# Kernel tuning notes

Hardware: AMD Instinct MI355X
Metric: run time of the kernel (lower is better)

## Reference

```python
import jax, jax.numpy as jnp
import numpy as np

W, L, D = 4096, 32, 256
WORD_VOCAB, CHR_VOCAB = 50000, 128


def conv1d(x, w, b):
    # x: [N, C_in, T], w: [C_out, C_in, 3], padding=1 (same)
    y = jax.lax.conv_general_dilated(
        x, w, window_strides=(1,), padding=[(1, 1)],
        dimension_numbers=("NCW", "OIW", "NCW"))
    return y + b[None, :, None]


def setup_inputs() -> dict:
    key = jax.random.key(0)
    ks = jax.random.split(key, 12)
    words = jax.random.randint(ks[0], (W,), 0, WORD_VOCAB, dtype=jnp.int32)
    words_in_char = jax.random.randint(ks[1], (W, L), 0, CHR_VOCAB, dtype=jnp.int32)
    s = 0.02
    word_emb = (jax.random.normal(ks[2], (WORD_VOCAB, D), jnp.float32) * s).at[0].set(0.0)  # padding_idx=0
    chr_emb = (jax.random.normal(ks[3], (CHR_VOCAB, D), jnp.float32) * s).at[0].set(0.0)
    conv_chr_w = jax.random.normal(ks[4], (D, D, 3), jnp.float32) * s
    conv_chr_b = jax.random.normal(ks[5], (D,), jnp.float32) * s
    conv_sent_w = jax.random.normal(ks[6], (2 * D, 2 * D, 3), jnp.float32) * s
    conv_sent_b = jax.random.normal(ks[7], (2 * D,), jnp.float32) * s
    w1 = jax.random.normal(ks[8], (4 * D, 2 * D), jnp.float32) * s
    b1 = jax.random.normal(ks[9], (4 * D,), jnp.float32) * s
    w2 = jax.random.normal(ks[10], (2, 4 * D), jnp.float32) * s
    b2 = jax.random.normal(ks[11], (2,), jnp.float32) * s
    return dict(words=words, words_in_char=words_in_char,
                word_emb=word_emb, chr_emb=chr_emb,
                conv_chr_w=conv_chr_w, conv_chr_b=conv_chr_b,
                conv_sent_w=conv_sent_w, conv_sent_b=conv_sent_b,
                w1=w1, b1=b1, w2=w2, b2=b2)


def reference(words, words_in_char, word_emb, chr_emb,
              conv_chr_w, conv_chr_b, conv_sent_w, conv_sent_b,
              w1, b1, w2, b2):
    # word embeddings: [W, D]
    vector_wrds = word_emb[words]
    # char path, batched over all words (equivalent to the per-word loop):
    ch = chr_emb[words_in_char]                      # [W, L, D]
    ch = jnp.transpose(ch, (0, 2, 1))                # [W, D, L]
    wc = conv1d(ch, conv_chr_w, conv_chr_b)          # [W, D, L]
    vector_wchs = jnp.max(wc, axis=2)                # [W, D]
    # sentence conv over the word axis
    u = jnp.concatenate([vector_wrds, vector_wchs], axis=1)  # [W, 2D]
    u = u.T[None, :, :]                              # [1, 2D, W]
    r = conv1d(u, conv_sent_w, conv_sent_b)          # [1, 2D, W]
    r = jnp.max(r, axis=2)                           # [1, 2D]
    h = jnp.tanh(r @ w1.T + b1)                      # [1, 4D]
    return h @ w2.T + b2                             # [1, 2]
```

## Files before the change

kernel.cpp:

```cpp
#include <hip/hip_runtime.h>
#include <hip/hip_bf16.h>
#include <math.h>

#define NW 4096
#define NL 32
#define ND 256
#define ND2 512

typedef __attribute__((ext_vector_type(8))) short short8;
typedef __attribute__((ext_vector_type(4))) float floatx4;

__device__ inline float bitsf(unsigned u) {
  union { unsigned u; float f; } v;
  v.u = u;
  return v.f;
}


__global__ __launch_bounds__(256) void prep_table_kernel(
    const float* __restrict__ conv_sent_w, const float* __restrict__ conv_chr_w,
    const float* __restrict__ chr_emb, __hip_bfloat16* __restrict__ Wb,
    __hip_bfloat16* __restrict__ Tb, short* __restrict__ u_base) {
  __shared__ float s_w[256][49];
  __shared__ float s_e[2][256];
  const int b = blockIdx.x;
  const int tid = threadIdx.x;
  if (b >= 64) {
    if (b < 3136) {
      int idx = (b - 64) * 256 + tid;
      float v = conv_sent_w[idx];
      int co = idx / 1536;
      int rem = idx - co * 1536;
      int ci = rem / 3;
      int k = rem - ci * 3;
      Wb[k * 262144 + co * 512 + ci] = __float2bfloat16(v);
    } else {
      u_base[tid] = 0; u_base[tid + 256] = 0;
      u_base[4097 * 512 + tid] = 0; u_base[4097 * 512 + tid + 256] = 0;
    }
    return;
  }
  const int c0 = b * 2;
  const int co = tid;
  s_e[0][tid] = chr_emb[(c0 + 0) * 256 + tid];
  s_e[1][tid] = chr_emb[(c0 + 1) * 256 + tid];
  float acc[2][3] = {};
  for (int chk = 0; chk < 16; ++chk) {
    const int ci0 = chk * 16;
    __syncthreads();
#pragma unroll 8
    for (int i = 0; i < 48; ++i) {
      int f = tid + i * 256;
      int wco = f / 48;
      int j = f - wco * 48;
      s_w[wco][j] = conv_chr_w[wco * 768 + ci0 * 3 + j];
    }
    __syncthreads();
#pragma unroll
    for (int ci = 0; ci < 16; ++ci) {
      float t_w0 = s_w[co][ci * 3 + 0];
      float t_w1 = s_w[co][ci * 3 + 1];
      float t_w2 = s_w[co][ci * 3 + 2];
      float e0 = s_e[0][ci0 + ci];
      float e1 = s_e[1][ci0 + ci];
      acc[0][0] = fmaf(e0, t_w0, acc[0][0]);
      acc[0][1] = fmaf(e0, t_w1, acc[0][1]);
      acc[0][2] = fmaf(e0, t_w2, acc[0][2]);
      acc[1][0] = fmaf(e1, t_w0, acc[1][0]);
      acc[1][1] = fmaf(e1, t_w1, acc[1][1]);
      acc[1][2] = fmaf(e1, t_w2, acc[1][2]);
    }
  }
  const int tbase = ((co >> 6) * 3) * 8192 + (co & 63);
#pragma unroll
  for (int k = 0; k < 3; ++k) {
    Tb[tbase + k * 8192 + (c0 + 0) * 64] = __float2bfloat16(acc[0][k]);
    Tb[tbase + k * 8192 + (c0 + 1) * 64] = __float2bfloat16(acc[1][k]);
  }
}

__global__ __launch_bounds__(256) void char_word_kernel(
    const int* __restrict__ words, const int* __restrict__ wic,
    const __hip_bfloat16* __restrict__ Tb, const float* __restrict__ word_emb,
    const float* __restrict__ bias, __hip_bfloat16* __restrict__ u0) {
  __shared__ short sT[3 * 128 * 64];
  __shared__ int s_wic[32 * 32];
  __shared__ int s_wid[32];
  const int ct = blockIdx.x >> 7;
  const int w0 = (blockIdx.x & 127) * 32;
  const int tid = threadIdx.x;
  {
    const uint4* src = (const uint4*)((const short*)Tb + ct * 24576);
    uint4* dst = (uint4*)sT;
#pragma unroll
    for (int i = 0; i < 12; ++i) dst[tid + i * 256] = src[tid + i * 256];
    ((int4*)s_wic)[tid] = ((const int4*)(wic + w0 * 32))[tid];
    if (tid < 32) s_wid[tid] = words[w0 + tid];
  }
  __syncthreads();
  {
    const int co_l = tid & 63, slot = tid >> 6;
#pragma unroll
    for (int wi = 0; wi < 8; ++wi) {
      int wl = slot * 8 + wi;
      u0[(w0 + wl) * ND2 + ct * 64 + co_l] =
          __float2bfloat16(word_emb[s_wid[wl] * ND + ct * 64 + co_l]);
    }
  }
  const int wave = tid >> 6, lane = tid & 63;
  const int half = lane >> 5, co2 = (lane & 31) * 2;
  const float2 bb = *(const float2*)&bias[ct * 64 + co2];
  const short* T0p = sT;
  const short* T1p = sT + 8192;
  const short* T2p = sT + 16384;
#pragma unroll
  for (int p = 0; p < 4; ++p) {
    const int wl = wave * 8 + p * 2 + half;
    int chv[32];
    const int4* c4 = (const int4*)(s_wic + wl * 32);
#pragma unroll
    for (int j = 0; j < 8; ++j) {
      int4 cc = c4[j];
      chv[4 * j + 0] = cc.x; chv[4 * j + 1] = cc.y;
      chv[4 * j + 2] = cc.z; chv[4 * j + 3] = cc.w;
    }
    float m0 = -INFINITY, m1 = -INFINITY;
#pragma unroll
    for (int t = 0; t < NL; ++t) {
      unsigned v1 = *(const unsigned*)&T1p[chv[t] * 64 + co2];
      float s0 = bitsf(v1 << 16);
      float s1 = bitsf(v1 & 0xffff0000u);
      if (t > 0) {
        unsigned v0 = *(const unsigned*)&T0p[chv[t - 1] * 64 + co2];
        s0 += bitsf(v0 << 16);
        s1 += bitsf(v0 & 0xffff0000u);
      }
      if (t < NL - 1) {
        unsigned v2 = *(const unsigned*)&T2p[chv[t + 1] * 64 + co2];
        s0 += bitsf(v2 << 16);
        s1 += bitsf(v2 & 0xffff0000u);
      }
      m0 = fmaxf(m0, s0);
      m1 = fmaxf(m1, s1);
    }
    __hip_bfloat162 hh;
    hh.x = __float2bfloat16(m0 + bb.x);
    hh.y = __float2bfloat16(m1 + bb.y);
    *(__hip_bfloat162*)&u0[(w0 + wl) * ND2 + ND + ct * 64 + co2] = hh;
  }
}

__global__ __launch_bounds__(256, 2) void sent_conv_mfma(
    const __hip_bfloat16* __restrict__ u0,
    const __hip_bfloat16* __restrict__ Wb,
    float* __restrict__ partial) {
  __shared__ short As[64 * 64];
  __shared__ short Bs[64 * 64];
  __shared__ float sm[4][32];
  const int tid = threadIdx.x;
  const int t0 = blockIdx.x * 64;
  const int co0 = blockIdx.y * 64;
  const int wave = tid >> 6, lane = tid & 63;
  const int wy = wave >> 1, wx = wave & 1;
  const int m = lane & 15, q = lane >> 4;

  floatx4 acc[2][2];
#pragma unroll
  for (int i = 0; i < 2; ++i)
#pragma unroll
    for (int j = 0; j < 2; ++j) acc[i][j] = (floatx4){0.f, 0.f, 0.f, 0.f};

  int aoff[2][2], boff[2][2];
#pragma unroll
  for (int kk = 0; kk < 2; ++kk) {
#pragma unroll
    for (int i = 0; i < 2; ++i) {
      int row = wy * 32 + i * 16 + m;
      aoff[kk][i] = row * 64 + (((kk * 4 + q) ^ (row & 7)) * 8);
      row = wx * 32 + i * 16 + m;
      boff[kk][i] = row * 64 + (((kk * 4 + q) ^ (row & 7)) * 8);
    }
  }

  const int sc = tid & 7, sr = tid >> 3;
  const int swc = (sc ^ (sr & 7)) * 8;
  const short* WbS = (const short*)Wb;
  const short* uS = (const short*)u0;

  for (int s = 0; s < 24; ++s) {
    int k = s >> 3, ci0 = (s & 7) << 6;
    const short* WbK = WbS + k * 262144 + (co0 + sr) * 512 + ci0 + sc * 8;
    const short* uK = uS + (t0 + sr + k - 1) * 512 + ci0 + sc * 8;
    uint4 a0 = *(const uint4*)(WbK);
    uint4 a1 = *(const uint4*)(WbK + 32 * 512);
    uint4 b0 = *(const uint4*)(uK);
    uint4 b1 = *(const uint4*)(uK + 32 * 512);
    *(uint4*)&As[sr * 64 + swc] = a0;
    *(uint4*)&As[(sr + 32) * 64 + swc] = a1;
    *(uint4*)&Bs[sr * 64 + swc] = b0;
    *(uint4*)&Bs[(sr + 32) * 64 + swc] = b1;
    __syncthreads();
#pragma unroll
    for (int kk = 0; kk < 2; ++kk) {
      short8 av0 = *(const short8*)&As[aoff[kk][0]];
      short8 av1 = *(const short8*)&As[aoff[kk][1]];
      short8 bv0 = *(const short8*)&Bs[boff[kk][0]];
      short8 bv1 = *(const short8*)&Bs[boff[kk][1]];
      acc[0][0] = __builtin_amdgcn_mfma_f32_16x16x32_bf16(av0, bv0, acc[0][0], 0, 0, 0);
      acc[0][1] = __builtin_amdgcn_mfma_f32_16x16x32_bf16(av0, bv1, acc[0][1], 0, 0, 0);
      acc[1][0] = __builtin_amdgcn_mfma_f32_16x16x32_bf16(av1, bv0, acc[1][0], 0, 0, 0);
      acc[1][1] = __builtin_amdgcn_mfma_f32_16x16x32_bf16(av1, bv1, acc[1][1], 0, 0, 0);
    }
    __syncthreads();
  }

#pragma unroll
  for (int i = 0; i < 2; ++i)
#pragma unroll
    for (int r = 0; r < 4; ++r) {
      float x = fmaxf(acc[i][0][r], acc[i][1][r]);
#pragma unroll
      for (int off = 1; off < 16; off <<= 1)
        x = fmaxf(x, __shfl_xor(x, off, 64));
      if (m == 0) sm[wave][i * 16 + q * 4 + r] = x;
    }
  __syncthreads();
  if (tid < 64) {
    int whalf = tid >> 5;
    float v = fmaxf(sm[whalf * 2 + 0][tid & 31], sm[whalf * 2 + 1][tid & 31]);
    partial[(co0 + tid) * 64 + blockIdx.x] = v;
  }
}

__global__ __launch_bounds__(512) void fc1_kernel(
    const float* __restrict__ partial, const float* __restrict__ bs,
    const float* __restrict__ w1, const float* __restrict__ b1,
    float* __restrict__ h) {
  __shared__ float s_r[512];
  int tid = threadIdx.x;
  {
    const float4* p = (const float4*)(partial + tid * 64);
    float mm = -INFINITY;
#pragma unroll
    for (int j = 0; j < 16; ++j) {
      float4 v = p[j];
      mm = fmaxf(mm, fmaxf(fmaxf(v.x, v.y), fmaxf(v.z, v.w)));
    }
    s_r[tid] = mm + bs[tid];
  }
  __syncthreads();
  int wave = tid >> 6, lane = tid & 63;
  int o = blockIdx.x * 8 + wave;
  const float4* wv = (const float4*)(w1 + o * 512 + lane * 8);
  const float4* rv = (const float4*)(s_r + lane * 8);
  float4 w0 = wv[0], w1v = wv[1];
  float4 r0 = rv[0], r1 = rv[1];
  float acc = w0.x * r0.x + w0.y * r0.y + w0.z * r0.z + w0.w * r0.w +
              w1v.x * r1.x + w1v.y * r1.y + w1v.z * r1.z + w1v.w * r1.w;
#pragma unroll
  for (int off = 32; off >= 1; off >>= 1) acc += __shfl_down(acc, off, 64);
  if (lane == 0) h[o] = tanhf(acc + b1[o]);
}

__global__ __launch_bounds__(128) void fc2_kernel(
    const float* __restrict__ h, const float* __restrict__ w2,
    const float* __restrict__ b2, float* __restrict__ out) {
  int tid = threadIdx.x;
  int o = tid >> 6;
  int lane = tid & 63;
  float acc = 0.f;
#pragma unroll
  for (int j = 0; j < 16; ++j)
    acc = fmaf(w2[o * 1024 + lane + j * 64], h[lane + j * 64], acc);
#pragma unroll
  for (int off = 32; off >= 1; off >>= 1) acc += __shfl_down(acc, off, 64);
  if (lane == 0) out[o] = acc + b2[o];
}

extern "C" void kernel_launch(void* const* d_in, const int* in_sizes, int n_in,
                              void* d_out, int out_size, void* d_ws, size_t ws_size,
                              hipStream_t stream) {
  const int*   words       = (const int*)d_in[0];
  const int*   wic         = (const int*)d_in[1];
  const float* word_emb    = (const float*)d_in[2];
  const float* chr_emb     = (const float*)d_in[3];
  const float* conv_chr_w  = (const float*)d_in[4];
  const float* conv_chr_b  = (const float*)d_in[5];
  const float* conv_sent_w = (const float*)d_in[6];
  const float* conv_sent_b = (const float*)d_in[7];
  const float* w1          = (const float*)d_in[8];
  const float* b1          = (const float*)d_in[9];
  const float* w2          = (const float*)d_in[10];
  const float* b2          = (const float*)d_in[11];
  float* out = (float*)d_out;

  float* ws    = (float*)d_ws;
  float* part  = ws;
  float* h_buf = part + 32768;
  short* Tb    = (short*)(h_buf + 1024);
  short* u_base = Tb + 98304;
  __hip_bfloat16* u0 = (__hip_bfloat16*)(u_base + 512);
  __hip_bfloat16* Wb = (__hip_bfloat16*)(u_base + 4098 * 512);

  prep_table_kernel<<<3137, 256, 0, stream>>>(conv_sent_w, conv_chr_w, chr_emb,
                                              Wb, (__hip_bfloat16*)Tb, u_base);
  char_word_kernel<<<512, 256, 0, stream>>>(words, wic, (const __hip_bfloat16*)Tb,
                                            word_emb, conv_chr_b, u0);
  sent_conv_mfma<<<dim3(64, 8), 256, 0, stream>>>(u0, Wb, part);
  fc1_kernel<<<128, 512, 0, stream>>>(part, conv_sent_b, w1, b1, h_buf);
  fc2_kernel<<<1, 128, 0, stream>>>(h_buf, w2, b2, out);
}
```

Before: 184.7 us.

## Split char table precompute via transposed weights; fuse fc2 into fc1 with atomic counter

The char-conv lookup table build is restructured. The prep kernel now transposes conv_chr_w into a [k][ci][co] fp32 buffer, and a new 96-block table kernel computes the embedding-times-weight products with coalesced weight reads, replacing the 64-block kernel that staged weights through shared memory with strided loads. Separately, fc2 is folded into fc1: the last block to finish, detected by an agent-scope atomic counter, computes the final two outputs, which removes one kernel launch. This adds a launch for the table kernel and a workspace counter that must be reset on every call.

```diff
diff --git a/kernel.cpp b/kernel.cpp
--- a/kernel.cpp
+++ b/kernel.cpp
@@ -17,66 +17,62 @@
 }
 
 
-__global__ __launch_bounds__(256) void prep_table_kernel(
+__global__ __launch_bounds__(256) void prep_kernel(
     const float* __restrict__ conv_sent_w, const float* __restrict__ conv_chr_w,
-    const float* __restrict__ chr_emb, __hip_bfloat16* __restrict__ Wb,
-    __hip_bfloat16* __restrict__ Tb, short* __restrict__ u_base) {
-  __shared__ float s_w[256][49];
-  __shared__ float s_e[2][256];
-  const int b = blockIdx.x;
-  const int tid = threadIdx.x;
-  if (b >= 64) {
-    if (b < 3136) {
-      int idx = (b - 64) * 256 + tid;
-      float v = conv_sent_w[idx];
-      int co = idx / 1536;
-      int rem = idx - co * 1536;
-      int ci = rem / 3;
-      int k = rem - ci * 3;
-      Wb[k * 262144 + co * 512 + ci] = __float2bfloat16(v);
-    } else {
-      u_base[tid] = 0; u_base[tid + 256] = 0;
-      u_base[4097 * 512 + tid] = 0; u_base[4097 * 512 + tid + 256] = 0;
-    }
-    return;
-  }
-  const int c0 = b * 2;
-  const int co = tid;
-  s_e[0][tid] = chr_emb[(c0 + 0) * 256 + tid];
-  s_e[1][tid] = chr_emb[(c0 + 1) * 256 + tid];
-  float acc[2][3] = {};
-  for (int chk = 0; chk < 16; ++chk) {
-    const int ci0 = chk * 16;
-    __syncthreads();
+    float* __restrict__ wT, __hip_bfloat16* __restrict__ Wb,
+    short* __restrict__ u_base, int* __restrict__ ctr) {
+  int b = blockIdx.x;
+  int tid = threadIdx.x;
+  if (b < 3072) {
+    int idx = b * 256 + tid;
+    float v = conv_sent_w[idx];
+    int co = idx / 1536;
+    int rem = idx - co * 1536;
+    int ci = rem / 3;
+    int k = rem - ci * 3;
+    Wb[k * 262144 + co * 512 + ci] = __float2bfloat16(v);
+  } else if (b < 3840) {
+    int idx = (b - 3072) * 256 + tid;
+    float v = conv_chr_w[idx];
+    int co = idx / 768;
+    int rem = idx - co * 768;
+    int ci = rem / 3;
+    int k = rem - ci * 3;
+    wT[k * 65536 + ci * 256 + co] = v;
+  } else {
+    u_base[tid] = 0;
+    u_base[tid + 256] = 0;
+    u_base[4097 * 512 + tid] = 0;
+    u_base[4097 * 512 + tid + 256] = 0;
+    if (tid == 0) ctr[0] = 0;
+  }
+}
+
+__global__ __launch_bounds__(256) void table_kernel(
+    const float* __restrict__ chr_emb, const float* __restrict__ wT,
+    __hip_bfloat16* __restrict__ Tb) {
+  __shared__ float s_e[4][256];
+  int k = blockIdx.x >> 5;
+  int c0 = (blockIdx.x & 31) * 4;
+  int co = threadIdx.x;
+#pragma unroll
+  for (int j = 0; j < 4; ++j) s_e[j][co] = chr_emb[(c0 + j) * 256 + co];
+  __syncthreads();
+  const float* wk = wT + k * 65536;
+  float a0 = 0.f, a1 = 0.f, a2 = 0.f, a3 = 0.f;
 #pragma unroll 8
-    for (int i = 0; i < 48; ++i) {
-      int f = tid + i * 256;
-      int wco = f / 48;
-      int j = f - wco * 48;
-      s_w[wco][j] = conv_chr_w[wco * 768 + ci0 * 3 + j];
-    }
-    __syncthreads();
-#pragma unroll
-    for (int ci = 0; ci < 16; ++ci) {
-      float t_w0 = s_w[co][ci * 3 + 0];
-      float t_w1 = s_w[co][ci * 3 + 1];
-      float t_w2 = s_w[co][ci * 3 + 2];
-      float e0 = s_e[0][ci0 + ci];
-      float e1 = s_e[1][ci0 + ci];
-      acc[0][0] = fmaf(e0, t_w0, acc[0][0]);
-      acc[0][1] = fmaf(e0, t_w1, acc[0][1]);
-      acc[0][2] = fmaf(e0, t_w2, acc[0][2]);
-      acc[1][0] = fmaf(e1, t_w0, acc[1][0]);
-      acc[1][1] = fmaf(e1, t_w1, acc[1][1]);
-      acc[1][2] = fmaf(e1, t_w2, acc[1][2]);
-    }
-  }
-  const int tbase = ((co >> 6) * 3) * 8192 + (co & 63);
-#pragma unroll
-  for (int k = 0; k < 3; ++k) {
-    Tb[tbase + k * 8192 + (c0 + 0) * 64] = __float2bfloat16(acc[0][k]);
-    Tb[tbase + k * 8192 + (c0 + 1) * 64] = __float2bfloat16(acc[1][k]);
-  }
+  for (int ci = 0; ci < 256; ++ci) {
+    float w = wk[ci * 256 + co];
+    a0 = fmaf(s_e[0][ci], w, a0);
+    a1 = fmaf(s_e[1][ci], w, a1);
+    a2 = fmaf(s_e[2][ci], w, a2);
+    a3 = fmaf(s_e[3][ci], w, a3);
+  }
+  int base = ((co >> 6) * 3 + k) * 8192 + (co & 63);
+  Tb[base + (c0 + 0) * 64] = __float2bfloat16(a0);
+  Tb[base + (c0 + 1) * 64] = __float2bfloat16(a1);
+  Tb[base + (c0 + 2) * 64] = __float2bfloat16(a2);
+  Tb[base + (c0 + 3) * 64] = __float2bfloat16(a3);
 }
 
 __global__ __launch_bounds__(256) void char_word_kernel(
@@ -232,11 +228,13 @@
   }
 }
 
-__global__ __launch_bounds__(512) void fc1_kernel(
+__global__ __launch_bounds__(512) void fc12_kernel(
     const float* __restrict__ partial, const float* __restrict__ bs,
     const float* __restrict__ w1, const float* __restrict__ b1,
-    float* __restrict__ h) {
+    const float* __restrict__ w2, const float* __restrict__ b2,
+    float* __restrict__ h, int* __restrict__ ctr, float* __restrict__ out) {
   __shared__ float s_r[512];
+  __shared__ int s_last;
   int tid = threadIdx.x;
   {
     const float4* p = (const float4*)(partial + tid * 64);
@@ -260,21 +258,27 @@
 #pragma unroll
   for (int off = 32; off >= 1; off >>= 1) acc += __shfl_down(acc, off, 64);
   if (lane == 0) h[o] = tanhf(acc + b1[o]);
-}
-
-__global__ __launch_bounds__(128) void fc2_kernel(
-    const float* __restrict__ h, const float* __restrict__ w2,
-    const float* __restrict__ b2, float* __restrict__ out) {
-  int tid = threadIdx.x;
-  int o = tid >> 6;
-  int lane = tid & 63;
-  float acc = 0.f;
-#pragma unroll
-  for (int j = 0; j < 16; ++j)
-    acc = fmaf(w2[o * 1024 + lane + j * 64], h[lane + j * 64], acc);
-#pragma unroll
-  for (int off = 32; off >= 1; off >>= 1) acc += __shfl_down(acc, off, 64);
-  if (lane == 0) out[o] = acc + b2[o];
+  __syncthreads();
+  if (tid == 0) {
+    int old = __hip_atomic_fetch_add(ctr, 1, __ATOMIC_RELEASE,
+                                     __HIP_MEMORY_SCOPE_AGENT);
+    s_last = (old == 127) ? 1 : 0;
+  }
+  __syncthreads();
+  if (s_last) {
+    __builtin_amdgcn_fence(__ATOMIC_ACQUIRE, "agent");
+    if (tid < 128) {
+      int o2 = tid >> 6;
+      int lane2 = tid & 63;
+      float acc2 = 0.f;
+#pragma unroll
+      for (int j = 0; j < 16; ++j)
+        acc2 = fmaf(w2[o2 * 1024 + lane2 + j * 64], h[lane2 + j * 64], acc2);
+#pragma unroll
+      for (int off = 32; off >= 1; off >>= 1) acc2 += __shfl_down(acc2, off, 64);
+      if (lane2 == 0) out[o2] = acc2 + b2[o2];
+    }
+  }
 }
 
 extern "C" void kernel_launch(void* const* d_in, const int* in_sizes, int n_in,
@@ -295,18 +299,21 @@
   float* out = (float*)d_out;
 
   float* ws    = (float*)d_ws;
-  float* part  = ws;
+  float* wT    = ws;
+  float* part  = wT + 196608;
   float* h_buf = part + 32768;
-  short* Tb    = (short*)(h_buf + 1024);
+  int*   ctr   = (int*)(h_buf + 1024);
+  short* Tb    = (short*)(ctr + 4);
   short* u_base = Tb + 98304;
   __hip_bfloat16* u0 = (__hip_bfloat16*)(u_base + 512);
   __hip_bfloat16* Wb = (__hip_bfloat16*)(u_base + 4098 * 512);
 
-  prep_table_kernel<<<3137, 256, 0, stream>>>(conv_sent_w, conv_chr_w, chr_emb,
-                                              Wb, (__hip_bfloat16*)Tb, u_base);
+  prep_kernel<<<3841, 256, 0, stream>>>(conv_sent_w, conv_chr_w, wT, Wb,
+                                        u_base, ctr);
+  table_kernel<<<96, 256, 0, stream>>>(chr_emb, wT, (__hip_bfloat16*)Tb);
   char_word_kernel<<<512, 256, 0, stream>>>(words, wic, (const __hip_bfloat16*)Tb,
                                             word_emb, conv_chr_b, u0);
   sent_conv_mfma<<<dim3(64, 8), 256, 0, stream>>>(u0, Wb, part);
-  fc1_kernel<<<128, 512, 0, stream>>>(part, conv_sent_b, w1, b1, h_buf);
-  fc2_kernel<<<1, 128, 0, stream>>>(h_buf, w2, b2, out);
-}
+  fc12_kernel<<<128, 512, 0, stream>>>(part, conv_sent_b, w1, b1, w2, b2,
+                                       h_buf, ctr, out);
+}
```

After: 158.1 us. 1.17x faster.
